# Kernel optimization log

Hardware: AMD Instinct MI355X
Metric: run time of the kernel (lower is better)

Reference implementation:

```python
import jax, jax.numpy as jnp
import numpy as np

C = 16          # cardinality (hard-coded in GraphHead)
E = 1024        # node_encoding_size == representation_size (residual requires equality)
S = 1024        # spatial_head output size (hard-coded Linear(256,1024))
R = 1024        # representation_size
D = R // C      # sub_repr_size = 64
NS, NO = 64, 256
NUM_ITER = 2
EPS = 1e-5


def _w(key, shape, fan_in):
    return jax.random.normal(key, shape, dtype=jnp.float32) * np.float32((2.0 / fan_in) ** 0.5)


def setup_inputs() -> dict:
    key = jax.random.key(0)
    ks = jax.random.split(key, 16)
    inp = {
        'h': jax.random.normal(ks[0], (NS, E), dtype=jnp.float32),
        'o': jax.random.normal(ks[1], (NO, E), dtype=jnp.float32),
        'spatial': jax.random.normal(ks[2], (NS, NO, S), dtype=jnp.float32),
        # attention_head: MultiBranchFusion(2E, 1024, R, 16)
        'att_w1': _w(ks[3], (C, 2 * E, D), 2 * E), 'att_b1': jnp.zeros((C, D), jnp.float32),
        'att_w2': _w(ks[4], (C, S, D), S),         'att_b2': jnp.zeros((C, D), jnp.float32),
        'att_w3': _w(ks[5], (C, D, R), D),         'att_b3': jnp.zeros((C, R), jnp.float32),
        # sub_to_obj: MessageMBF(E, 1024, R, 'subject', 16)
        's2o_w1': _w(ks[6], (C, E, D), E),         's2o_b1': jnp.zeros((C, D), jnp.float32),
        's2o_w2': _w(ks[7], (C, S, D), S),         's2o_b2': jnp.zeros((C, D), jnp.float32),
        's2o_w3': _w(ks[8], (C, D, R), D),         's2o_b3': jnp.zeros((C, R), jnp.float32),
        # obj_to_sub: MessageMBF(E, 1024, R, 'object', 16)
        'o2s_w1': _w(ks[9], (C, E, D), E),         'o2s_b1': jnp.zeros((C, D), jnp.float32),
        'o2s_w2': _w(ks[10], (C, S, D), S),        'o2s_b2': jnp.zeros((C, D), jnp.float32),
        'o2s_w3': _w(ks[11], (C, D, R), D),        'o2s_b3': jnp.zeros((C, R), jnp.float32),
        # adjacency: Linear(R, 1)
        'adj_w': _w(ks[12], (R, 1), R), 'adj_b': jnp.zeros((1,), jnp.float32),
        # LayerNorms
        'ns_g': jnp.ones((E,), jnp.float32), 'ns_b': jnp.zeros((E,), jnp.float32),
        'no_g': jnp.ones((E,), jnp.float32), 'no_b': jnp.zeros((E,), jnp.float32),
    }
    return inp


def _layernorm(x, g, b):
    m = jnp.mean(x, axis=-1, keepdims=True)
    v = jnp.mean((x - m) ** 2, axis=-1, keepdims=True)
    return (x - m) * jax.lax.rsqrt(v + EPS) * g + b


def _mbf_pair(app, spa, w1, b1, w2, b2, w3, b3):
    # app [ns,no,A], spa [ns,no,S] -> [ns,no,R]; sum over C branches of fc3(relu(fc1*fc2))
    a = jnp.einsum('ija,cad->cijd', app, w1) + b1[:, None, None, :]
    s = jnp.einsum('ijs,csd->cijd', spa, w2) + b2[:, None, None, :]
    g = jax.nn.relu(a * s)
    return jnp.einsum('cijd,cdr->ijr', g, w3) + b3.sum(0)


def _msg_subject(h, spa, w1, b1, w2, b2, w3, b3):
    # MessageMBF subject: broadcast fc1(h) [ns,d] against fc2(spa) [ns,no,d]
    a = jnp.einsum('ia,cad->cid', h, w1) + b1[:, None, :]
    s = jnp.einsum('ijs,csd->cijd', spa, w2) + b2[:, None, None, :]
    g = jax.nn.relu(a[:, :, None, :] * s)
    return jnp.einsum('cijd,cdr->ijr', g, w3) + b3.sum(0)  # [ns,no,R]


def _msg_object(o, spa, w1, b1, w2, b2, w3, b3):
    # MessageMBF object: broadcast fc1(o) [no,d] against fc2(spa) [ns,no,d]
    a = jnp.einsum('ja,cad->cjd', o, w1) + b1[:, None, :]
    s = jnp.einsum('ijs,csd->cijd', spa, w2) + b2[:, None, None, :]
    g = jax.nn.relu(a[:, None, :, :] * s)
    return jnp.einsum('cijd,cdr->ijr', g, w3) + b3.sum(0)  # [ns,no,R]


def reference(h, o, spatial,
              att_w1, att_b1, att_w2, att_b2, att_w3, att_b3,
              s2o_w1, s2o_b1, s2o_w2, s2o_b2, s2o_w3, s2o_b3,
              o2s_w1, o2s_b1, o2s_w2, o2s_b2, o2s_w3, o2s_b3,
              adj_w, adj_b, ns_g, ns_b, no_g, no_b):
    ns, no = h.shape[0], o.shape[0]
    for _ in range(NUM_ITER):
        # edge weights via attention MBF on concatenated pair encodings
        pair_app = jnp.concatenate([
            jnp.broadcast_to(h[:, None, :], (ns, no, E)),
            jnp.broadcast_to(o[None, :, :], (ns, no, E)),
        ], axis=-1)
        w = jax.nn.relu(_mbf_pair(pair_app, spatial, att_w1, att_b1, att_w2, att_b2, att_w3, att_b3))
        adj = jnp.einsum('ijr,rk->ij', w, adj_w) + adj_b[0]  # [ns,no]
        # update subject nodes from object messages
        m_o2s = _msg_object(o, spatial, o2s_w1, o2s_b1, o2s_w2, o2s_b2, o2s_w3, o2s_b3)
        msg_h = jax.nn.relu(jnp.einsum('ij,ijr->ir', jax.nn.softmax(adj, axis=1), m_o2s))
        h = _layernorm(h + msg_h, ns_g, ns_b)
        # update object nodes from (updated) subject messages
        m_s2o = _msg_subject(h, spatial, s2o_w1, s2o_b1, s2o_w2, s2o_b2, s2o_w3, s2o_b3)
        msg_o = jax.nn.relu(jnp.einsum('ij,ijr->jr', jax.nn.softmax(adj, axis=0), m_s2o))
        o = _layernorm(o + msg_o, no_g, no_b)
    return jnp.concatenate([h, o], axis=0)  # [ns+no, E]
```

## Files before the change

### kernel.cpp

```cpp
#include <hip/hip_runtime.h>
#include <cstdint>
#include <cstddef>

typedef _Float16 hf;
typedef _Float16 h8v __attribute__((ext_vector_type(8)));
typedef float f4v __attribute__((ext_vector_type(4)));

#define NS 64
#define NO 256
#define MP 16384
#define KD 1024

__device__ __forceinline__ h8v cvt8(float4 a, float4 b) {
    h8v r;
    r[0] = (hf)a.x; r[1] = (hf)a.y; r[2] = (hf)a.z; r[3] = (hf)a.w;
    r[4] = (hf)b.x; r[5] = (hf)b.y; r[6] = (hf)b.z; r[7] = (hf)b.w;
    return r;
}
__device__ __forceinline__ float f4at(const float4& a, const float4& b, int e) {
    const float* p = e < 4 ? (const float*)&a : (const float*)&b;
    return p[e & 3];
}

__global__ void k_pack16(const float* __restrict__ src, hf* __restrict__ dst, int n8) {
    int g = blockIdx.x * 256 + threadIdx.x;
    if (g >= n8) return;
    const float4* s4 = (const float4*)src;
    float4 a = s4[2 * g], b = s4[2 * g + 1];
    *(h8v*)(dst + (size_t)g * 8) = cvt8(a, b);
}

struct RoR { const float* src; hf* dhi; hf* dlo; int Asrc; int aOff; };
struct RoRs { RoR r[7]; };
__global__ void k_reorder16b(RoRs RR) {
    const RoR rt = RR.r[blockIdx.z];
    __shared__ float tile[64][65];
    int c = blockIdx.x, a0 = blockIdx.y * 64;
    int t = threadIdx.x, lx = t & 63, ly = t >> 6;
#pragma unroll
    for (int p = 0; p < 16; ++p) {
        int ar = ly + p * 4;
        tile[ar][lx] = rt.src[(size_t)(c * rt.Asrc + rt.aOff + a0 + ar) * 64 + lx];
    }
    __syncthreads();
#pragma unroll
    for (int p = 0; p < 16; ++p) {
        int d = ly + p * 4;
        float v = tile[lx][d];
        hf h = (hf)v;
        size_t idx = (size_t)(c * 64 + d) * 1024 + a0 + lx;
        rt.dhi[idx] = h;
        if (rt.dlo) rt.dlo[idx] = (hf)(v - (float)h);
    }
}

struct TrR { const float* src; hf* dhi; hf* dlo; };
struct TrRs { TrR r[3]; };
__global__ void k_transpose16b(TrRs RR) {
    const TrR rt = RR.r[blockIdx.z];
    __shared__ float tile[64][65];
    int r0 = blockIdx.x * 64, s0 = blockIdx.y * 64;
    int t = threadIdx.x, lx = t & 63, ly = t >> 6;
#pragma unroll
    for (int p = 0; p < 16; ++p) {
        int srow = ly + p * 4;
        tile[srow][lx] = rt.src[(size_t)(s0 + srow) * 1024 + r0 + lx];
    }
    __syncthreads();
#pragma unroll
    for (int p = 0; p < 16; ++p) {
        int rr = ly + p * 4;
        float v = tile[lx][rr];
        hf h = (hf)v;
        size_t idx = (size_t)(r0 + rr) * 1024 + s0 + lx;
        rt.dhi[idx] = h;
        if (rt.dlo) rt.dlo[idx] = (hf)(v - (float)h);
    }
}

__global__ void k_prep_bc(const float* __restrict__ ab2, const float* __restrict__ ob2,
                          const float* __restrict__ sb2, const float* __restrict__ ab3,
                          const float* __restrict__ ob3, const float* __restrict__ sb3,
                          float* __restrict__ b2cat, float* __restrict__ b3a,
                          float* __restrict__ b3o, float* __restrict__ b3s) {
    int g = blockIdx.x * 256 + threadIdx.x;
    if (g >= 1024) return;
    b2cat[g] = ab2[g]; b2cat[1024 + g] = ob2[g]; b2cat[2048 + g] = sb2[g];
    float sa = 0.f, so = 0.f, ss = 0.f;
    for (int c = 0; c < 16; ++c) {
        sa += ab3[c * 1024 + g];
        so += ob3[c * 1024 + g];
        ss += sb3[c * 1024 + g];
    }
    b3a[g] = sa; b3o[g] = so; b3s[g] = ss;
}

__global__ void k_init_ho(const float* __restrict__ h, const float* __restrict__ o,
                          float* __restrict__ outbuf, hf* __restrict__ h16, hf* __restrict__ o16) {
    int g = blockIdx.x * 256 + threadIdx.x;
    if (g < NS * KD) { float v = h[g]; outbuf[g] = v; h16[g] = (hf)v; }
    int g2 = g - NS * KD;
    if (g2 >= 0 && g2 < NO * KD) { float v = o[g2]; outbuf[NS * KD + g2] = v; o16[g2] = (hf)v; }
}

__global__ __launch_bounds__(256, 2) void k_prep_gemm(
    const hf* __restrict__ sp16,
    const hf* __restrict__ Wah, const hf* __restrict__ Wal,
    const hf* __restrict__ Wo2, const hf* __restrict__ Ws2,
    const float* __restrict__ b2cat,
    hf* __restrict__ Sh, hf* __restrict__ Sl,
    hf* __restrict__ So, hf* __restrict__ Ss) {
    __shared__ hf Ah[4096];
    __shared__ hf Bh[8192];
    __shared__ hf Bl[8192];
    const int tid = threadIdx.x;
    int lin = blockIdx.y * 12 + blockIdx.x;
    int xcd = lin & 7, slot = lin >> 3;
    int xn = slot % 12;
    const int m0 = ((xcd << 4) + slot / 12) * 128;
    const int plane = xn >> 2;
    const int nbase = (xn & 3) * 256;
    const hf* Bb = plane == 0 ? Wah : (plane == 1 ? Wo2 : Ws2);
    const bool hasL = (plane == 0);
    const int lane = tid & 63, wid = tid >> 6;
    const int wm = wid >> 1, wn = wid & 1;
    const int lr = lane & 15, lg = lane >> 4;
    const int srow = tid >> 2, sseg = tid & 3;
    const int wo_ = srow * 32 + (sseg ^ ((srow >> 1) & 3)) * 8;
    const int rsl = (lg ^ ((lr >> 1) & 3)) * 8;

    f4v acc[2][4][4];
    f4v zz; zz[0] = 0.f; zz[1] = 0.f; zz[2] = 0.f; zz[3] = 0.f;
#pragma unroll
    for (int u = 0; u < 2; ++u)
#pragma unroll
        for (int a = 0; a < 4; ++a)
#pragma unroll
            for (int b = 0; b < 4; ++b) acc[u][a][b] = zz;

    const int ko = sseg * 8;
    const hf* pa0 = sp16 + (size_t)(m0 + srow) * KD + ko;
    const hf* pa1 = sp16 + (size_t)(m0 + 64 + srow) * KD + ko;
    const hf* pb00 = Bb + (size_t)(nbase + srow) * KD + ko;
    const hf* pb01 = Bb + (size_t)(nbase + 64 + srow) * KD + ko;
    const hf* pb10 = Bb + (size_t)(nbase + 128 + srow) * KD + ko;
    const hf* pb11 = Bb + (size_t)(nbase + 192 + srow) * KD + ko;
    const hf* ql00 = Wal + (size_t)(nbase + srow) * KD + ko;
    const hf* ql01 = Wal + (size_t)(nbase + 64 + srow) * KD + ko;
    const hf* ql10 = Wal + (size_t)(nbase + 128 + srow) * KD + ko;
    const hf* ql11 = Wal + (size_t)(nbase + 192 + srow) * KD + ko;

    h8v va0, va1, vb00, vb01, vb10, vb11, wb00, wb01, wb10, wb11;
    auto LOAD = [&](int kk) {
        va0 = *(const h8v*)(pa0 + kk); va1 = *(const h8v*)(pa1 + kk);
        vb00 = *(const h8v*)(pb00 + kk); vb01 = *(const h8v*)(pb01 + kk);
        vb10 = *(const h8v*)(pb10 + kk); vb11 = *(const h8v*)(pb11 + kk);
        if (hasL) {
            wb00 = *(const h8v*)(ql00 + kk); wb01 = *(const h8v*)(ql01 + kk);
            wb10 = *(const h8v*)(ql10 + kk); wb11 = *(const h8v*)(ql11 + kk);
        }
    };
    LOAD(0);
    for (int t = 0; t < 32; ++t) {
        __syncthreads();
        *(h8v*)(Ah + wo_) = va0; *(h8v*)(Ah + 2048 + wo_) = va1;
        *(h8v*)(Bh + wo_) = vb00; *(h8v*)(Bh + 2048 + wo_) = vb01;
        *(h8v*)(Bh + 4096 + wo_) = vb10; *(h8v*)(Bh + 6144 + wo_) = vb11;
        if (hasL) {
            *(h8v*)(Bl + wo_) = wb00; *(h8v*)(Bl + 2048 + wo_) = wb01;
            *(h8v*)(Bl + 4096 + wo_) = wb10; *(h8v*)(Bl + 6144 + wo_) = wb11;
        }
        __syncthreads();
        if (t + 1 < 32) LOAD((t + 1) * 32);
        h8v fa[4], fb[4];
#pragma unroll
        for (int x = 0; x < 4; ++x)
            fa[x] = *(const h8v*)(Ah + (wm * 64 + x * 16 + lr) * 32 + rsl);
#pragma unroll
        for (int u = 0; u < 2; ++u) {
#pragma unroll
            for (int x = 0; x < 4; ++x)
                fb[x] = *(const h8v*)(Bh + u * 4096 + (wn * 64 + x * 16 + lr) * 32 + rsl);
#pragma unroll
            for (int mi = 0; mi < 4; ++mi)
#pragma unroll
                for (int ni = 0; ni < 4; ++ni)
                    acc[u][mi][ni] = __builtin_amdgcn_mfma_f32_16x16x32_f16(fa[mi], fb[ni], acc[u][mi][ni], 0, 0, 0);
            if (hasL) {
#pragma unroll
                for (int x = 0; x < 4; ++x)
                    fb[x] = *(const h8v*)(Bl + u * 4096 + (wn * 64 + x * 16 + lr) * 32 + rsl);
#pragma unroll
                for (int mi = 0; mi < 4; ++mi)
#pragma unroll
                    for (int ni = 0; ni < 4; ++ni)
                        acc[u][mi][ni] = __builtin_amdgcn_mfma_f32_16x16x32_f16(fa[mi], fb[ni], acc[u][mi][ni], 0, 0, 0);
            }
        }
    }
#pragma unroll
    for (int u = 0; u < 2; ++u)
#pragma unroll
        for (int mi = 0; mi < 4; ++mi)
#pragma unroll
            for (int ni = 0; ni < 4; ++ni)
#pragma unroll
                for (int r = 0; r < 4; ++r) {
                    int gr = m0 + wm * 64 + mi * 16 + lg * 4 + r;
                    int col = nbase + u * 128 + wn * 64 + ni * 16 + lr;
                    float v = acc[u][mi][ni][r] + b2cat[plane * 1024 + col];
                    size_t idx = (size_t)gr * KD + col;
                    if (plane == 0) {
                        hf hi = (hf)v;
                        Sh[idx] = hi; Sl[idx] = (hf)(v - (float)hi);
                    } else if (plane == 1) So[idx] = (hf)v;
                    else Ss[idx] = (hf)v;
                }
}

__global__ void k_build_g(const hf* __restrict__ Sh, const hf* __restrict__ Sl,
                          const float* __restrict__ e1, const float* __restrict__ e2,
                          hf* __restrict__ Gh, hf* __restrict__ Gl) {
    int g = blockIdx.x * 256 + threadIdx.x;
    size_t base = (size_t)g * 8;
    int m = (int)(base >> 10);
    int k = (int)(base & 1023);
    int i = m >> 8, j = m & 255;
    h8v sh = *(const h8v*)(Sh + base);
    h8v sl = *(const h8v*)(Sl + base);
    float4 ex0 = *(const float4*)(e1 + (size_t)i * KD + k);
    float4 ex1 = *(const float4*)(e1 + (size_t)i * KD + k + 4);
    float4 ey0 = *(const float4*)(e2 + (size_t)j * KD + k);
    float4 ey1 = *(const float4*)(e2 + (size_t)j * KD + k + 4);
    h8v gh, gl;
#pragma unroll
    for (int e = 0; e < 8; ++e) {
        float s = (float)sh[e] + (float)sl[e];
        float ee = f4at(ex0, ex1, e) + f4at(ey0, ey1, e);
        float gg = ee * s; gg = gg > 0.f ? gg : 0.f;
        hf hi = (hf)gg; gh[e] = hi; gl[e] = (hf)(gg - (float)hi);
    }
    *(h8v*)(Gh + base) = gh;
    *(h8v*)(Gl + base) = gl;
}

__global__ __launch_bounds__(256, 2) void k_adj_gemm(
    const hf* __restrict__ Gh, const hf* __restrict__ Gl,
    const hf* __restrict__ W3h, const hf* __restrict__ W3l,
    const float* __restrict__ b3, const float* __restrict__ aw,
    float* __restrict__ adjv) {
    __shared__ hf Ah[4096];
    __shared__ hf Al[4096];
    __shared__ hf Bh[8192];
    __shared__ hf Bl[8192];
    const int tid = threadIdx.x;
    int lin = blockIdx.y * 4 + blockIdx.x;
    int xcd = lin & 7, slot = lin >> 3;
    const int nbase = (slot & 3) * 256;
    const int m0 = ((xcd << 4) + (slot >> 2)) * 128;
    const int lane = tid & 63, wid = tid >> 6;
    const int wm = wid >> 1, wn = wid & 1;
    const int lr = lane & 15, lg = lane >> 4;
    const int srow = tid >> 2, sseg = tid & 3;
    const int wo_ = srow * 32 + (sseg ^ ((srow >> 1) & 3)) * 8;
    const int rsl = (lg ^ ((lr >> 1) & 3)) * 8;
    const int ar0 = m0 + srow, ar1 = ar0 + 64;
    const int ko = sseg * 8;

    f4v acc[2][4][4];
    f4v zz; zz[0] = 0.f; zz[1] = 0.f; zz[2] = 0.f; zz[3] = 0.f;
#pragma unroll
    for (int u = 0; u < 2; ++u)
#pragma unroll
        for (int a = 0; a < 4; ++a)
#pragma unroll
            for (int b = 0; b < 4; ++b) acc[u][a][b] = zz;

    h8v va0, va1, ua0, ua1;
    h8v vb00, vb01, vb10, vb11, wb00, wb01, wb10, wb11;
    auto LOAD = [&](int kk) {
        va0 = *(const h8v*)(Gh + (size_t)ar0 * KD + ko + kk);
        va1 = *(const h8v*)(Gh + (size_t)ar1 * KD + ko + kk);
        ua0 = *(const h8v*)(Gl + (size_t)ar0 * KD + ko + kk);
        ua1 = *(const h8v*)(Gl + (size_t)ar1 * KD + ko + kk);
        vb00 = *(const h8v*)(W3h + (size_t)(nbase + srow) * KD + ko + kk);
        vb01 = *(const h8v*)(W3h + (size_t)(nbase + 64 + srow) * KD + ko + kk);
        vb10 = *(const h8v*)(W3h + (size_t)(nbase + 128 + srow) * KD + ko + kk);
        vb11 = *(const h8v*)(W3h + (size_t)(nbase + 192 + srow) * KD + ko + kk);
        wb00 = *(const h8v*)(W3l + (size_t)(nbase + srow) * KD + ko + kk);
        wb01 = *(const h8v*)(W3l + (size_t)(nbase + 64 + srow) * KD + ko + kk);
        wb10 = *(const h8v*)(W3l + (size_t)(nbase + 128 + srow) * KD + ko + kk);
        wb11 = *(const h8v*)(W3l + (size_t)(nbase + 192 + srow) * KD + ko + kk);
    };
    LOAD(0);
    for (int t = 0; t < 32; ++t) {
        __syncthreads();
        *(h8v*)(Ah + wo_) = va0; *(h8v*)(Ah + 2048 + wo_) = va1;
        *(h8v*)(Al + wo_) = ua0; *(h8v*)(Al + 2048 + wo_) = ua1;
        *(h8v*)(Bh + wo_) = vb00; *(h8v*)(Bh + 2048 + wo_) = vb01;
        *(h8v*)(Bh + 4096 + wo_) = vb10; *(h8v*)(Bh + 6144 + wo_) = vb11;
        *(h8v*)(Bl + wo_) = wb00; *(h8v*)(Bl + 2048 + wo_) = wb01;
        *(h8v*)(Bl + 4096 + wo_) = wb10; *(h8v*)(Bl + 6144 + wo_) = wb11;
        __syncthreads();
        if (t + 1 < 32) LOAD((t + 1) * 32);
        h8v fa[4], fal[4], fb[4];
#pragma unroll
        for (int x = 0; x < 4; ++x) {
            fa[x]  = *(const h8v*)(Ah + (wm * 64 + x * 16 + lr) * 32 + rsl);
            fal[x] = *(const h8v*)(Al + (wm * 64 + x * 16 + lr) * 32 + rsl);
        }
#pragma unroll
        for (int u = 0; u < 2; ++u) {
#pragma unroll
            for (int x = 0; x < 4; ++x)
                fb[x] = *(const h8v*)(Bh + u * 4096 + (wn * 64 + x * 16 + lr) * 32 + rsl);
#pragma unroll
            for (int mi = 0; mi < 4; ++mi)
#pragma unroll
                for (int ni = 0; ni < 4; ++ni)
                    acc[u][mi][ni] = __builtin_amdgcn_mfma_f32_16x16x32_f16(fa[mi], fb[ni], acc[u][mi][ni], 0, 0, 0);
#pragma unroll
            for (int mi = 0; mi < 4; ++mi)
#pragma unroll
                for (int ni = 0; ni < 4; ++ni)
                    acc[u][mi][ni] = __builtin_amdgcn_mfma_f32_16x16x32_f16(fal[mi], fb[ni], acc[u][mi][ni], 0, 0, 0);
#pragma unroll
            for (int x = 0; x < 4; ++x)
                fb[x] = *(const h8v*)(Bl + u * 4096 + (wn * 64 + x * 16 + lr) * 32 + rsl);
#pragma unroll
            for (int mi = 0; mi < 4; ++mi)
#pragma unroll
                for (int ni = 0; ni < 4; ++ni)
                    acc[u][mi][ni] = __builtin_amdgcn_mfma_f32_16x16x32_f16(fa[mi], fb[ni], acc[u][mi][ni], 0, 0, 0);
        }
    }
    float b3v[2][4], awv[2][4];
#pragma unroll
    for (int u = 0; u < 2; ++u)
#pragma unroll
        for (int ni = 0; ni < 4; ++ni) {
            int gc = nbase + u * 128 + wn * 64 + ni * 16 + lr;
            b3v[u][ni] = b3[gc]; awv[u][ni] = aw[gc];
        }
#pragma unroll
    for (int mi = 0; mi < 4; ++mi)
#pragma unroll
        for (int r = 0; r < 4; ++r) {
            float part = 0.f;
#pragma unroll
            for (int u = 0; u < 2; ++u)
#pragma unroll
                for (int ni = 0; ni < 4; ++ni) {
                    float w = acc[u][mi][ni][r] + b3v[u][ni];
                    w = w > 0.f ? w : 0.f;
                    part += w * awv[u][ni];
                }
            part += __shfl_xor(part, 1);
            part += __shfl_xor(part, 2);
            part += __shfl_xor(part, 4);
            part += __shfl_xor(part, 8);
            if (lr == 0) atomicAdd(adjv + m0 + wm * 64 + mi * 16 + lg * 4 + r, part);
        }
}

struct SRoute { const hf* A; const hf* Bh; const hf* Bl; float* C; const float* bias; int m0; int M; };
struct SRoutes { SRoute r[5]; };

__global__ __launch_bounds__(256) void k_small(SRoutes RR) {
    const SRoute rt = RR.r[blockIdx.y];
    __shared__ hf Ah[4096];
    __shared__ hf Bh[4096];
    __shared__ hf Bl[4096];
    const int tid = threadIdx.x;
    const int n0 = blockIdx.x * 128;
    const int kbeg = blockIdx.z * 128;
    const int lane = tid & 63, wid = tid >> 6;
    const int wm = wid >> 1, wn = wid & 1;
    const int lr = lane & 15, lg = lane >> 4;
    const int srow = tid >> 2, sseg = tid & 3;
    const int wo_ = srow * 32 + (sseg ^ ((srow >> 1) & 3)) * 8;
    const int rsl = (lg ^ ((lr >> 1) & 3)) * 8;
    int ar0 = rt.m0 + srow;      if (ar0 >= rt.M) ar0 = rt.M - 1;
    int ar1 = rt.m0 + 64 + srow; if (ar1 >= rt.M) ar1 = rt.M - 1;
    const bool hasL = rt.Bl != nullptr;
    const int ko = kbeg + sseg * 8;

    f4v acc[4][4];
    f4v zz; zz[0] = 0.f; zz[1] = 0.f; zz[2] = 0.f; zz[3] = 0.f;
#pragma unroll
    for (int a = 0; a < 4; ++a)
#pragma unroll
        for (int b = 0; b < 4; ++b) acc[a][b] = zz;

    h8v va0, va1, vb0, vb1, wb0, wb1;
    auto LOAD = [&](int kk) {
        va0 = *(const h8v*)(rt.A + (size_t)ar0 * KD + ko + kk);
        va1 = *(const h8v*)(rt.A + (size_t)ar1 * KD + ko + kk);
        vb0 = *(const h8v*)(rt.Bh + (size_t)(n0 + srow) * KD + ko + kk);
        vb1 = *(const h8v*)(rt.Bh + (size_t)(n0 + 64 + srow) * KD + ko + kk);
        if (hasL) {
            wb0 = *(const h8v*)(rt.Bl + (size_t)(n0 + srow) * KD + ko + kk);
            wb1 = *(const h8v*)(rt.Bl + (size_t)(n0 + 64 + srow) * KD + ko + kk);
        }
    };
    LOAD(0);
    for (int t = 0; t < 4; ++t) {
        __syncthreads();
        *(h8v*)(Ah + wo_) = va0; *(h8v*)(Ah + 2048 + wo_) = va1;
        *(h8v*)(Bh + wo_) = vb0; *(h8v*)(Bh + 2048 + wo_) = vb1;
        if (hasL) { *(h8v*)(Bl + wo_) = wb0; *(h8v*)(Bl + 2048 + wo_) = wb1; }
        __syncthreads();
        if (t + 1 < 4) LOAD((t + 1) * 32);
        h8v fa[4], fb[4];
#pragma unroll
        for (int x = 0; x < 4; ++x) {
            fa[x] = *(const h8v*)(Ah + (wm * 64 + x * 16 + lr) * 32 + rsl);
            fb[x] = *(const h8v*)(Bh + (wn * 64 + x * 16 + lr) * 32 + rsl);
        }
#pragma unroll
        for (int mi = 0; mi < 4; ++mi)
#pragma unroll
            for (int ni = 0; ni < 4; ++ni)
                acc[mi][ni] = __builtin_amdgcn_mfma_f32_16x16x32_f16(fa[mi], fb[ni], acc[mi][ni], 0, 0, 0);
        if (hasL) {
#pragma unroll
            for (int x = 0; x < 4; ++x)
                fb[x] = *(const h8v*)(Bl + (wn * 64 + x * 16 + lr) * 32 + rsl);
#pragma unroll
            for (int mi = 0; mi < 4; ++mi)
#pragma unroll
                for (int ni = 0; ni < 4; ++ni)
                    acc[mi][ni] = __builtin_amdgcn_mfma_f32_16x16x32_f16(fa[mi], fb[ni], acc[mi][ni], 0, 0, 0);
        }
    }
#pragma unroll
    for (int mi = 0; mi < 4; ++mi)
#pragma unroll
        for (int ni = 0; ni < 4; ++ni)
#pragma unroll
            for (int r = 0; r < 4; ++r) {
                int gr = rt.m0 + wm * 64 + mi * 16 + lg * 4 + r;
                int gc = n0 + wn * 64 + ni * 16 + lr;
                if (gr < rt.M) {
                    float v = acc[mi][ni][r];
                    if (rt.bias && blockIdx.z == 0) v += rt.bias[gc];
                    atomicAdd(rt.C + (size_t)gr * KD + gc, v);
                }
            }
}

__global__ void k_softmax_rows(const float* __restrict__ adj, float* __restrict__ p) {
    __shared__ float red[256];
    int i = blockIdx.x, j = threadIdx.x;
    float x = adj[i * 256 + j];
    red[j] = x; __syncthreads();
    for (int s = 128; s > 0; s >>= 1) { if (j < s) red[j] = fmaxf(red[j], red[j + s]); __syncthreads(); }
    float mx = red[0]; __syncthreads();
    float e = __expf(x - mx);
    red[j] = e; __syncthreads();
    for (int s = 128; s > 0; s >>= 1) { if (j < s) red[j] += red[j + s]; __syncthreads(); }
    p[i * 256 + j] = e / red[0];
}

__global__ void k_softmax_cols(const float* __restrict__ adj, float* __restrict__ q) {
    int j = blockIdx.x, i = threadIdx.x;
    float x = adj[i * 256 + j];
    float mx = x;
#pragma unroll
    for (int off = 32; off > 0; off >>= 1) mx = fmaxf(mx, __shfl_xor(mx, off));
    float e = __expf(x - mx);
    float s = e;
#pragma unroll
    for (int off = 32; off > 0; off >>= 1) s += __shfl_xor(s, off);
    q[i * 256 + j] = e / s;
}

__global__ void k_build_Gh(const hf* __restrict__ S, const float* __restrict__ aF,
                           const float* __restrict__ p, hf* __restrict__ Gh) {
    __shared__ float pl[256];
    int i = blockIdx.x;
    int k = blockIdx.y * 256 + threadIdx.x;
    pl[threadIdx.x] = p[i * 256 + threadIdx.x];
    __syncthreads();
    const hf* sp = S + (size_t)(i * 256) * KD + k;
    float acc = 0.f;
#pragma unroll 4
    for (int j = 0; j < 256; ++j) {
        float a = aF[(size_t)j * KD + k];
        float s = (float)sp[(size_t)j * KD];
        float g = a * s; g = g > 0.f ? g : 0.f;
        acc += pl[j] * g;
    }
    Gh[(size_t)i * KD + k] = (hf)acc;
}

__global__ void k_build_Go(const hf* __restrict__ S, const float* __restrict__ aF,
                           const float* __restrict__ q, hf* __restrict__ Go) {
    __shared__ float ql[64];
    int j = blockIdx.x;
    int k = blockIdx.y * 256 + threadIdx.x;
    if (threadIdx.x < 64) ql[threadIdx.x] = q[threadIdx.x * 256 + j];
    __syncthreads();
    const hf* sp = S + (size_t)j * KD + k;
    float acc = 0.f;
#pragma unroll 4
    for (int i = 0; i < 64; ++i) {
        float a = aF[(size_t)i * KD + k];
        float s = (float)sp[(size_t)(i * 256) * KD];
        float g = a * s; g = g > 0.f ? g : 0.f;
        acc += ql[i] * g;
    }
    Go[(size_t)j * KD + k] = (hf)acc;
}

__global__ void k_ln_update(float* __restrict__ x, const float* __restrict__ msg,
                            const float* __restrict__ b3, const float* __restrict__ gamma,
                            const float* __restrict__ beta, hf* __restrict__ x16) {
    __shared__ float red[256];
    int r = blockIdx.x, t = threadIdx.x;
    float v[4];
    float s = 0.f;
#pragma unroll
    for (int e = 0; e < 4; ++e) {
        int idx = t + e * 256;
        float mm = msg[(size_t)r * KD + idx] + b3[idx];
        mm = mm > 0.f ? mm : 0.f;
        v[e] = x[(size_t)r * KD + idx] + mm;
        s += v[e];
    }
    red[t] = s; __syncthreads();
    for (int st = 128; st > 0; st >>= 1) { if (t < st) red[t] += red[t + st]; __syncthreads(); }
    float mean = red[0] * (1.f / 1024.f);
    __syncthreads();
    float s2 = 0.f;
#pragma unroll
    for (int e = 0; e < 4; ++e) { float d = v[e] - mean; s2 += d * d; }
    red[t] = s2; __syncthreads();
    for (int st = 128; st > 0; st >>= 1) { if (t < st) red[t] += red[t + st]; __syncthreads(); }
    float var = red[0] * (1.f / 1024.f);
    float rstd = rsqrtf(var + 1e-5f);
#pragma unroll
    for (int e = 0; e < 4; ++e) {
        int idx = t + e * 256;
        float y = (v[e] - mean) * rstd * gamma[idx] + beta[idx];
        x[(size_t)r * KD + idx] = y;
        x16[(size_t)r * KD + idx] = (hf)y;
    }
}

extern "C" void kernel_launch(void* const* d_in, const int* in_sizes, int n_in,
                              void* d_out, int out_size, void* d_ws, size_t ws_size,
                              hipStream_t stream) {
    const float* h_in    = (const float*)d_in[0];
    const float* o_in    = (const float*)d_in[1];
    const float* spatial = (const float*)d_in[2];
    const float* att_w1  = (const float*)d_in[3];
    const float* att_b1  = (const float*)d_in[4];
    const float* att_w2  = (const float*)d_in[5];
    const float* att_b2  = (const float*)d_in[6];
    const float* att_w3  = (const float*)d_in[7];
    const float* att_b3  = (const float*)d_in[8];
    const float* s2o_w1  = (const float*)d_in[9];
    const float* s2o_b1  = (const float*)d_in[10];
    const float* s2o_w2  = (const float*)d_in[11];
    const float* s2o_b2  = (const float*)d_in[12];
    const float* s2o_w3  = (const float*)d_in[13];
    const float* s2o_b3  = (const float*)d_in[14];
    const float* o2s_w1  = (const float*)d_in[15];
    const float* o2s_b1  = (const float*)d_in[16];
    const float* o2s_w2  = (const float*)d_in[17];
    const float* o2s_b2  = (const float*)d_in[18];
    const float* o2s_w3  = (const float*)d_in[19];
    const float* o2s_b3  = (const float*)d_in[20];
    const float* adj_w   = (const float*)d_in[21];
    const float* ns_g    = (const float*)d_in[23];
    const float* ns_b    = (const float*)d_in[24];
    const float* no_g    = (const float*)d_in[25];
    const float* no_b    = (const float*)d_in[26];

    char* ws = (char*)d_ws;
    size_t off = 0;
    auto alloc = [&](size_t bytes) -> char* {
        char* pp = ws + off;
        off += (bytes + 255) & ~(size_t)255;
        return pp;
    };
    const size_t PLANE = (size_t)MP * KD * sizeof(hf);
    const size_t WMAT  = (size_t)1024 * 1024 * sizeof(hf);
    hf* S_att_h = (hf*)alloc(PLANE);
    hf* S_att_l = (hf*)alloc(PLANE);
    hf* S_o2s   = (hf*)alloc(PLANE);
    hf* S_s2o   = (hf*)alloc(PLANE);
    hf* gA_h    = (hf*)alloc(PLANE);
    hf* gA_l    = (hf*)alloc(PLANE);
    hf* sp16    = gA_h;
    hf* W2att_h = (hf*)alloc(WMAT); hf* W2att_l = (hf*)alloc(WMAT);
    hf* W2o2s   = (hf*)alloc(WMAT);
    hf* W2s2o   = (hf*)alloc(WMAT);
    hf* W1ah_h  = (hf*)alloc(WMAT); hf* W1ah_l  = (hf*)alloc(WMAT);
    hf* W1ao_h  = (hf*)alloc(WMAT); hf* W1ao_l  = (hf*)alloc(WMAT);
    hf* W1o2s   = (hf*)alloc(WMAT);
    hf* W1s2o   = (hf*)alloc(WMAT);
    hf* W3a_h   = (hf*)alloc(WMAT); hf* W3a_l   = (hf*)alloc(WMAT);
    hf* W3o     = (hf*)alloc(WMAT);
    hf* W3s     = (hf*)alloc(WMAT);
    float* b2cat = (float*)alloc(3072 * 4);
    float* b3a   = (float*)alloc(1024 * 4);
    float* b3o   = (float*)alloc(1024 * 4);
    float* b3s   = (float*)alloc(1024 * 4);
    float* fc1h = (float*)alloc((size_t)NS * KD * 4);
    float* fc1o = (float*)alloc((size_t)NO * KD * 4);
    float* aO2S = (float*)alloc((size_t)NO * KD * 4);
    float* aS2O = (float*)alloc((size_t)NS * KD * 4);
    float* msgh = (float*)alloc((size_t)NS * KD * 4);
    float* msgo = (float*)alloc((size_t)NO * KD * 4);
    float* adjv = (float*)alloc((size_t)MP * 4);
    char* zend_ = (char*)(adjv + MP);
    size_t zlen = (size_t)(zend_ - (char*)fc1h);
    float* pbuf = (float*)alloc((size_t)MP * 4);
    float* qbuf = (float*)alloc((size_t)MP * 4);
    hf* h16 = (hf*)alloc((size_t)NS * KD * sizeof(hf));
    hf* o16 = (hf*)alloc((size_t)NO * KD * sizeof(hf));
    hf* Gh  = (hf*)alloc((size_t)NS * KD * sizeof(hf));
    hf* Go  = (hf*)alloc((size_t)NO * KD * sizeof(hf));

    float* hbuf = (float*)d_out;
    float* obuf = (float*)d_out + NS * KD;

    k_pack16<<<dim3(MP * KD / 8 / 256), 256, 0, stream>>>(spatial, sp16, MP * KD / 8);
    {
        RoRs R;
        R.r[0] = { att_w2, W2att_h, W2att_l, 1024, 0 };
        R.r[1] = { o2s_w2, W2o2s, nullptr, 1024, 0 };
        R.r[2] = { s2o_w2, W2s2o, nullptr, 1024, 0 };
        R.r[3] = { att_w1, W1ah_h, W1ah_l, 2048, 0 };
        R.r[4] = { att_w1, W1ao_h, W1ao_l, 2048, 1024 };
        R.r[5] = { o2s_w1, W1o2s, nullptr, 1024, 0 };
        R.r[6] = { s2o_w1, W1s2o, nullptr, 1024, 0 };
        k_reorder16b<<<dim3(16, 16, 7), 256, 0, stream>>>(R);
    }
    {
        TrRs T;
        T.r[0] = { att_w3, W3a_h, W3a_l };
        T.r[1] = { o2s_w3, W3o, nullptr };
        T.r[2] = { s2o_w3, W3s, nullptr };
        k_transpose16b<<<dim3(16, 16, 3), 256, 0, stream>>>(T);
    }
    k_prep_bc<<<dim3(4), 256, 0, stream>>>(att_b2, o2s_b2, s2o_b2, att_b3, o2s_b3, s2o_b3,
                                           b2cat, b3a, b3o, b3s);
    k_init_ho<<<dim3(1280), 256, 0, stream>>>(h_in, o_in, (float*)d_out, h16, o16);
    k_prep_gemm<<<dim3(12, 128), 256, 0, stream>>>(sp16, W2att_h, W2att_l, W2o2s, W2s2o,
                                                   b2cat, S_att_h, S_att_l, S_o2s, S_s2o);

    for (int it = 0; it < 2; ++it) {
        hipMemsetAsync(fc1h, 0, zlen, stream);
        {
            SRoutes R;
            R.r[0] = { h16, W1ah_h, W1ah_l, fc1h, att_b1, 0,   NS };
            R.r[1] = { o16, W1ao_h, W1ao_l, fc1o, nullptr, 0,   NO };
            R.r[2] = { o16, W1ao_h, W1ao_l, fc1o, nullptr, 128, NO };
            R.r[3] = { o16, W1o2s,  nullptr, aO2S, o2s_b1, 0,   NO };
            R.r[4] = { o16, W1o2s,  nullptr, aO2S, o2s_b1, 128, NO };
            k_small<<<dim3(8, 5, 8), 256, 0, stream>>>(R);
        }
        k_build_g<<<dim3(MP * KD / 8 / 256), 256, 0, stream>>>(S_att_h, S_att_l, fc1h, fc1o, gA_h, gA_l);
        k_adj_gemm<<<dim3(4, 128), 256, 0, stream>>>(gA_h, gA_l, W3a_h, W3a_l, b3a, adj_w, adjv);
        k_softmax_rows<<<dim3(NS), 256, 0, stream>>>(adjv, pbuf);
        k_softmax_cols<<<dim3(NO), 64, 0, stream>>>(adjv, qbuf);
        k_build_Gh<<<dim3(NS, 4), 256, 0, stream>>>(S_o2s, aO2S, pbuf, Gh);
        {
            SRoutes R;
            R.r[0] = { Gh, W3o, nullptr, msgh, nullptr, 0, NS };
            k_small<<<dim3(8, 1, 8), 256, 0, stream>>>(R);
        }
        k_ln_update<<<dim3(NS), 256, 0, stream>>>(hbuf, msgh, b3o, ns_g, ns_b, h16);
        {
            SRoutes R;
            R.r[0] = { h16, W1s2o, nullptr, aS2O, s2o_b1, 0, NS };
            k_small<<<dim3(8, 1, 8), 256, 0, stream>>>(R);
        }
        k_build_Go<<<dim3(NO, 4), 256, 0, stream>>>(S_s2o, aS2O, qbuf, Go);
        {
            SRoutes R;
            R.r[0] = { Go, W3s, nullptr, msgo, nullptr, 0,   NO };
            R.r[1] = { Go, W3s, nullptr, msgo, nullptr, 128, NO };
            k_small<<<dim3(8, 2, 8), 256, 0, stream>>>(R);
        }
        k_ln_update<<<dim3(NO), 256, 0, stream>>>(obuf, msgo, b3s, no_g, no_b, o16);
    }
    (void)in_sizes; (void)n_in; (void)out_size; (void)ws_size;
}
```

Baseline: 682.3 us.

## Double-buffer B tiles in LDS and load A fragments straight from global

In both the prep GEMM and the adjacency GEMM, the A operand is no longer staged through shared memory; each wave loads its MFMA A fragments directly from global memory. The B tiles are double-buffered in LDS, so each iteration needs one barrier instead of two and the next tile's store overlaps the current compute. This cuts LDS traffic and synchronisation, but A fragment loads are now uncoalesced per-row global reads issued right before use, which can expose latency. LDS use per block goes up.

```diff
diff --git a/kernel.cpp b/kernel.cpp
--- a/kernel.cpp
+++ b/kernel.cpp
@@ -110,9 +110,8 @@
     const float* __restrict__ b2cat,
     hf* __restrict__ Sh, hf* __restrict__ Sl,
     hf* __restrict__ So, hf* __restrict__ Ss) {
-    __shared__ hf Ah[4096];
-    __shared__ hf Bh[8192];
-    __shared__ hf Bl[8192];
+    __shared__ hf Bh[2][8192];
+    __shared__ hf Bl[2][8192];
     const int tid = threadIdx.x;
     int lin = blockIdx.y * 12 + blockIdx.x;
     int xcd = lin & 7, slot = lin >> 3;
@@ -139,8 +138,6 @@
             for (int b = 0; b < 4; ++b) acc[u][a][b] = zz;
 
     const int ko = sseg * 8;
-    const hf* pa0 = sp16 + (size_t)(m0 + srow) * KD + ko;
-    const hf* pa1 = sp16 + (size_t)(m0 + 64 + srow) * KD + ko;
     const hf* pb00 = Bb + (size_t)(nbase + srow) * KD + ko;
     const hf* pb01 = Bb + (size_t)(nbase + 64 + srow) * KD + ko;
     const hf* pb10 = Bb + (size_t)(nbase + 128 + srow) * KD + ko;
@@ -149,10 +146,13 @@
     const hf* ql01 = Wal + (size_t)(nbase + 64 + srow) * KD + ko;
     const hf* ql10 = Wal + (size_t)(nbase + 128 + srow) * KD + ko;
     const hf* ql11 = Wal + (size_t)(nbase + 192 + srow) * KD + ko;
-
-    h8v va0, va1, vb00, vb01, vb10, vb11, wb00, wb01, wb10, wb11;
-    auto LOAD = [&](int kk) {
-        va0 = *(const h8v*)(pa0 + kk); va1 = *(const h8v*)(pa1 + kk);
+    const hf* pA[4];
+#pragma unroll
+    for (int mi = 0; mi < 4; ++mi)
+        pA[mi] = sp16 + (size_t)(m0 + wm * 64 + mi * 16 + lr) * KD + lg * 8;
+
+    h8v vb00, vb01, vb10, vb11, wb00, wb01, wb10, wb11;
+    auto LOADB = [&](int kk) {
         vb00 = *(const h8v*)(pb00 + kk); vb01 = *(const h8v*)(pb01 + kk);
         vb10 = *(const h8v*)(pb10 + kk); vb11 = *(const h8v*)(pb11 + kk);
         if (hasL) {
@@ -160,27 +160,31 @@
             wb10 = *(const h8v*)(ql10 + kk); wb11 = *(const h8v*)(ql11 + kk);
         }
     };
-    LOAD(0);
+    auto STOREB = [&](int b) {
+        hf* B = Bh[b]; hf* BL = Bl[b];
+        *(h8v*)(B + wo_) = vb00; *(h8v*)(B + 2048 + wo_) = vb01;
+        *(h8v*)(B + 4096 + wo_) = vb10; *(h8v*)(B + 6144 + wo_) = vb11;
+        if (hasL) {
+            *(h8v*)(BL + wo_) = wb00; *(h8v*)(BL + 2048 + wo_) = wb01;
+            *(h8v*)(BL + 4096 + wo_) = wb10; *(h8v*)(BL + 6144 + wo_) = wb11;
+        }
+    };
+    LOADB(0);
+    STOREB(0);
+    __syncthreads();
     for (int t = 0; t < 32; ++t) {
-        __syncthreads();
-        *(h8v*)(Ah + wo_) = va0; *(h8v*)(Ah + 2048 + wo_) = va1;
-        *(h8v*)(Bh + wo_) = vb00; *(h8v*)(Bh + 2048 + wo_) = vb01;
-        *(h8v*)(Bh + 4096 + wo_) = vb10; *(h8v*)(Bh + 6144 + wo_) = vb11;
-        if (hasL) {
-            *(h8v*)(Bl + wo_) = wb00; *(h8v*)(Bl + 2048 + wo_) = wb01;
-            *(h8v*)(Bl + 4096 + wo_) = wb10; *(h8v*)(Bl + 6144 + wo_) = wb11;
-        }
-        __syncthreads();
-        if (t + 1 < 32) LOAD((t + 1) * 32);
-        h8v fa[4], fb[4];
-#pragma unroll
-        for (int x = 0; x < 4; ++x)
-            fa[x] = *(const h8v*)(Ah + (wm * 64 + x * 16 + lr) * 32 + rsl);
+        const int cur = t & 1;
+        if (t < 31) LOADB((t + 1) * 32);
+        h8v fa[4];
+#pragma unroll
+        for (int mi = 0; mi < 4; ++mi) fa[mi] = *(const h8v*)(pA[mi] + t * 32);
+        const hf* B = Bh[cur]; const hf* BL = Bl[cur];
+        h8v fb[4];
 #pragma unroll
         for (int u = 0; u < 2; ++u) {
 #pragma unroll
             for (int x = 0; x < 4; ++x)
-                fb[x] = *(const h8v*)(Bh + u * 4096 + (wn * 64 + x * 16 + lr) * 32 + rsl);
+                fb[x] = *(const h8v*)(B + u * 4096 + (wn * 64 + x * 16 + lr) * 32 + rsl);
 #pragma unroll
             for (int mi = 0; mi < 4; ++mi)
 #pragma unroll
@@ -189,7 +193,7 @@
             if (hasL) {
 #pragma unroll
                 for (int x = 0; x < 4; ++x)
-                    fb[x] = *(const h8v*)(Bl + u * 4096 + (wn * 64 + x * 16 + lr) * 32 + rsl);
+                    fb[x] = *(const h8v*)(BL + u * 4096 + (wn * 64 + x * 16 + lr) * 32 + rsl);
 #pragma unroll
                 for (int mi = 0; mi < 4; ++mi)
 #pragma unroll
@@ -197,6 +201,8 @@
                         acc[u][mi][ni] = __builtin_amdgcn_mfma_f32_16x16x32_f16(fa[mi], fb[ni], acc[u][mi][ni], 0, 0, 0);
             }
         }
+        if (t < 31) STOREB(cur ^ 1);
+        __syncthreads();
     }
 #pragma unroll
     for (int u = 0; u < 2; ++u)
@@ -249,10 +255,8 @@
     const hf* __restrict__ W3h, const hf* __restrict__ W3l,
     const float* __restrict__ b3, const float* __restrict__ aw,
     float* __restrict__ adjv) {
-    __shared__ hf Ah[4096];
-    __shared__ hf Al[4096];
-    __shared__ hf Bh[8192];
-    __shared__ hf Bl[8192];
+    __shared__ hf Bh2[2][8192];
+    __shared__ hf Bl2[2][8192];
     const int tid = threadIdx.x;
     int lin = blockIdx.y * 4 + blockIdx.x;
     int xcd = lin & 7, slot = lin >> 3;
@@ -264,7 +268,6 @@
     const int srow = tid >> 2, sseg = tid & 3;
     const int wo_ = srow * 32 + (sseg ^ ((srow >> 1) & 3)) * 8;
     const int rsl = (lg ^ ((lr >> 1) & 3)) * 8;
-    const int ar0 = m0 + srow, ar1 = ar0 + 64;
     const int ko = sseg * 8;
 
     f4v acc[2][4][4];
@@ -276,44 +279,54 @@
 #pragma unroll
             for (int b = 0; b < 4; ++b) acc[u][a][b] = zz;
 
-    h8v va0, va1, ua0, ua1;
+    const hf* pb00 = W3h + (size_t)(nbase + srow) * KD + ko;
+    const hf* pb01 = W3h + (size_t)(nbase + 64 + srow) * KD + ko;
+    const hf* pb10 = W3h + (size_t)(nbase + 128 + srow) * KD + ko;
+    const hf* pb11 = W3h + (size_t)(nbase + 192 + srow) * KD + ko;
+    const hf* ql00 = W3l + (size_t)(nbase + srow) * KD + ko;
+    const hf* ql01 = W3l + (size_t)(nbase + 64 + srow) * KD + ko;
+    const hf* ql10 = W3l + (size_t)(nbase + 128 + srow) * KD + ko;
+    const hf* ql11 = W3l + (size_t)(nbase + 192 + srow) * KD + ko;
+    const hf* pAh[4]; const hf* pAl[4];
+#pragma unroll
+    for (int mi = 0; mi < 4; ++mi) {
+        size_t roff = (size_t)(m0 + wm * 64 + mi * 16 + lr) * KD + lg * 8;
+        pAh[mi] = Gh + roff; pAl[mi] = Gl + roff;
+    }
+
     h8v vb00, vb01, vb10, vb11, wb00, wb01, wb10, wb11;
-    auto LOAD = [&](int kk) {
-        va0 = *(const h8v*)(Gh + (size_t)ar0 * KD + ko + kk);
-        va1 = *(const h8v*)(Gh + (size_t)ar1 * KD + ko + kk);
-        ua0 = *(const h8v*)(Gl + (size_t)ar0 * KD + ko + kk);
-        ua1 = *(const h8v*)(Gl + (size_t)ar1 * KD + ko + kk);
-        vb00 = *(const h8v*)(W3h + (size_t)(nbase + srow) * KD + ko + kk);
-        vb01 = *(const h8v*)(W3h + (size_t)(nbase + 64 + srow) * KD + ko + kk);
-        vb10 = *(const h8v*)(W3h + (size_t)(nbase + 128 + srow) * KD + ko + kk);
-        vb11 = *(const h8v*)(W3h + (size_t)(nbase + 192 + srow) * KD + ko + kk);
-        wb00 = *(const h8v*)(W3l + (size_t)(nbase + srow) * KD + ko + kk);
-        wb01 = *(const h8v*)(W3l + (size_t)(nbase + 64 + srow) * KD + ko + kk);
-        wb10 = *(const h8v*)(W3l + (size_t)(nbase + 128 + srow) * KD + ko + kk);
-        wb11 = *(const h8v*)(W3l + (size_t)(nbase + 192 + srow) * KD + ko + kk);
+    auto LOADB = [&](int kk) {
+        vb00 = *(const h8v*)(pb00 + kk); vb01 = *(const h8v*)(pb01 + kk);
+        vb10 = *(const h8v*)(pb10 + kk); vb11 = *(const h8v*)(pb11 + kk);
+        wb00 = *(const h8v*)(ql00 + kk); wb01 = *(const h8v*)(ql01 + kk);
+        wb10 = *(const h8v*)(ql10 + kk); wb11 = *(const h8v*)(ql11 + kk);
     };
-    LOAD(0);
+    auto STOREB = [&](int b) {
+        hf* B = Bh2[b]; hf* BL = Bl2[b];
+        *(h8v*)(B + wo_) = vb00; *(h8v*)(B + 2048 + wo_) = vb01;
+        *(h8v*)(B + 4096 + wo_) = vb10; *(h8v*)(B + 6144 + wo_) = vb11;
+        *(h8v*)(BL + wo_) = wb00; *(h8v*)(BL + 2048 + wo_) = wb01;
+        *(h8v*)(BL + 4096 + wo_) = wb10; *(h8v*)(BL + 6144 + wo_) = wb11;
+    };
+    LOADB(0);
+    STOREB(0);
+    __syncthreads();
     for (int t = 0; t < 32; ++t) {
-        __syncthreads();
-        *(h8v*)(Ah + wo_) = va0; *(h8v*)(Ah + 2048 + wo_) = va1;
-        *(h8v*)(Al + wo_) = ua0; *(h8v*)(Al + 2048 + wo_) = ua1;
-        *(h8v*)(Bh + wo_) = vb00; *(h8v*)(Bh + 2048 + wo_) = vb01;
-        *(h8v*)(Bh + 4096 + wo_) = vb10; *(h8v*)(Bh + 6144 + wo_) = vb11;
-        *(h8v*)(Bl + wo_) = wb00; *(h8v*)(Bl + 2048 + wo_) = wb01;
-        *(h8v*)(Bl + 4096 + wo_) = wb10; *(h8v*)(Bl + 6144 + wo_) = wb11;
-        __syncthreads();
-        if (t + 1 < 32) LOAD((t + 1) * 32);
-        h8v fa[4], fal[4], fb[4];
-#pragma unroll
-        for (int x = 0; x < 4; ++x) {
-            fa[x]  = *(const h8v*)(Ah + (wm * 64 + x * 16 + lr) * 32 + rsl);
-            fal[x] = *(const h8v*)(Al + (wm * 64 + x * 16 + lr) * 32 + rsl);
-        }
+        const int cur = t & 1;
+        if (t < 31) LOADB((t + 1) * 32);
+        h8v fa[4], fal[4];
+#pragma unroll
+        for (int mi = 0; mi < 4; ++mi) {
+            fa[mi]  = *(const h8v*)(pAh[mi] + t * 32);
+            fal[mi] = *(const h8v*)(pAl[mi] + t * 32);
+        }
+        const hf* B = Bh2[cur]; const hf* BL = Bl2[cur];
+        h8v fb[4];
 #pragma unroll
         for (int u = 0; u < 2; ++u) {
 #pragma unroll
             for (int x = 0; x < 4; ++x)
-                fb[x] = *(const h8v*)(Bh + u * 4096 + (wn * 64 + x * 16 + lr) * 32 + rsl);
+                fb[x] = *(const h8v*)(B + u * 4096 + (wn * 64 + x * 16 + lr) * 32 + rsl);
 #pragma unroll
             for (int mi = 0; mi < 4; ++mi)
 #pragma unroll
@@ -326,13 +339,15 @@
                     acc[u][mi][ni] = __builtin_amdgcn_mfma_f32_16x16x32_f16(fal[mi], fb[ni], acc[u][mi][ni], 0, 0, 0);
 #pragma unroll
             for (int x = 0; x < 4; ++x)
-                fb[x] = *(const h8v*)(Bl + u * 4096 + (wn * 64 + x * 16 + lr) * 32 + rsl);
+                fb[x] = *(const h8v*)(BL + u * 4096 + (wn * 64 + x * 16 + lr) * 32 + rsl);
 #pragma unroll
             for (int mi = 0; mi < 4; ++mi)
 #pragma unroll
                 for (int ni = 0; ni < 4; ++ni)
                     acc[u][mi][ni] = __builtin_amdgcn_mfma_f32_16x16x32_f16(fa[mi], fb[ni], acc[u][mi][ni], 0, 0, 0);
         }
+        if (t < 31) STOREB(cur ^ 1);
+        __syncthreads();
     }
     float b3v[2][4], awv[2][4];
 #pragma unroll
```

Measured after the change: 742.6 us. 1.09x slower.

## Double-buffer B tiles in LDS and load A fragments directly from global

Applied to the files above, without the earlier changes.

In the prep GEMM, the B tiles are now double-buffered in shared memory, so only one barrier per k-step is needed instead of two. The A operand no longer goes through LDS: each wave loads its MFMA fragments straight from global memory into registers, prefetched one step ahead. This removes the A staging stores and reads and overlaps the next B store with compute. In exchange, LDS use grows (two B buffers, 64KB total), which may limit occupancy. A global loads are also less coalesced and duplicated across the two wn waves.

```diff
diff --git a/kernel.cpp b/kernel.cpp
--- a/kernel.cpp
+++ b/kernel.cpp
@@ -110,9 +110,8 @@
     const float* __restrict__ b2cat,
     hf* __restrict__ Sh, hf* __restrict__ Sl,
     hf* __restrict__ So, hf* __restrict__ Ss) {
-    __shared__ hf Ah[4096];
-    __shared__ hf Bh[8192];
-    __shared__ hf Bl[8192];
+    __shared__ hf Bhs[2][8192];
+    __shared__ hf Bls[2][8192];
     const int tid = threadIdx.x;
     int lin = blockIdx.y * 12 + blockIdx.x;
     int xcd = lin & 7, slot = lin >> 3;
@@ -139,8 +138,6 @@
             for (int b = 0; b < 4; ++b) acc[u][a][b] = zz;
 
     const int ko = sseg * 8;
-    const hf* pa0 = sp16 + (size_t)(m0 + srow) * KD + ko;
-    const hf* pa1 = sp16 + (size_t)(m0 + 64 + srow) * KD + ko;
     const hf* pb00 = Bb + (size_t)(nbase + srow) * KD + ko;
     const hf* pb01 = Bb + (size_t)(nbase + 64 + srow) * KD + ko;
     const hf* pb10 = Bb + (size_t)(nbase + 128 + srow) * KD + ko;
@@ -149,10 +146,13 @@
     const hf* ql01 = Wal + (size_t)(nbase + 64 + srow) * KD + ko;
     const hf* ql10 = Wal + (size_t)(nbase + 128 + srow) * KD + ko;
     const hf* ql11 = Wal + (size_t)(nbase + 192 + srow) * KD + ko;
-
-    h8v va0, va1, vb00, vb01, vb10, vb11, wb00, wb01, wb10, wb11;
-    auto LOAD = [&](int kk) {
-        va0 = *(const h8v*)(pa0 + kk); va1 = *(const h8v*)(pa1 + kk);
+    const hf* pA[4];
+#pragma unroll
+    for (int mi = 0; mi < 4; ++mi)
+        pA[mi] = sp16 + (size_t)(m0 + wm * 64 + mi * 16 + lr) * KD + lg * 8;
+
+    h8v vb00, vb01, vb10, vb11, wb00, wb01, wb10, wb11;
+    auto LOADB = [&](int kk) {
         vb00 = *(const h8v*)(pb00 + kk); vb01 = *(const h8v*)(pb01 + kk);
         vb10 = *(const h8v*)(pb10 + kk); vb11 = *(const h8v*)(pb11 + kk);
         if (hasL) {
@@ -160,27 +160,38 @@
             wb10 = *(const h8v*)(ql10 + kk); wb11 = *(const h8v*)(ql11 + kk);
         }
     };
-    LOAD(0);
+    auto STOREB = [&](int b) {
+        hf* B = Bhs[b]; hf* BL = Bls[b];
+        *(h8v*)(B + wo_) = vb00; *(h8v*)(B + 2048 + wo_) = vb01;
+        *(h8v*)(B + 4096 + wo_) = vb10; *(h8v*)(B + 6144 + wo_) = vb11;
+        if (hasL) {
+            *(h8v*)(BL + wo_) = wb00; *(h8v*)(BL + 2048 + wo_) = wb01;
+            *(h8v*)(BL + 4096 + wo_) = wb10; *(h8v*)(BL + 6144 + wo_) = wb11;
+        }
+    };
+    h8v fan[4];
+    LOADB(0);
+#pragma unroll
+    for (int mi = 0; mi < 4; ++mi) fan[mi] = *(const h8v*)(pA[mi]);
+    STOREB(0);
+    __syncthreads();
     for (int t = 0; t < 32; ++t) {
-        __syncthreads();
-        *(h8v*)(Ah + wo_) = va0; *(h8v*)(Ah + 2048 + wo_) = va1;
-        *(h8v*)(Bh + wo_) = vb00; *(h8v*)(Bh + 2048 + wo_) = vb01;
-        *(h8v*)(Bh + 4096 + wo_) = vb10; *(h8v*)(Bh + 6144 + wo_) = vb11;
-        if (hasL) {
-            *(h8v*)(Bl + wo_) = wb00; *(h8v*)(Bl + 2048 + wo_) = wb01;
-            *(h8v*)(Bl + 4096 + wo_) = wb10; *(h8v*)(Bl + 6144 + wo_) = wb11;
-        }
-        __syncthreads();
-        if (t + 1 < 32) LOAD((t + 1) * 32);
-        h8v fa[4], fb[4];
-#pragma unroll
-        for (int x = 0; x < 4; ++x)
-            fa[x] = *(const h8v*)(Ah + (wm * 64 + x * 16 + lr) * 32 + rsl);
+        const int cur = t & 1;
+        h8v fa[4];
+#pragma unroll
+        for (int mi = 0; mi < 4; ++mi) fa[mi] = fan[mi];
+        if (t < 31) {
+            LOADB((t + 1) * 32);
+#pragma unroll
+            for (int mi = 0; mi < 4; ++mi) fan[mi] = *(const h8v*)(pA[mi] + (t + 1) * 32);
+        }
+        const hf* B = Bhs[cur]; const hf* BL = Bls[cur];
+        h8v fb[4];
 #pragma unroll
         for (int u = 0; u < 2; ++u) {
 #pragma unroll
             for (int x = 0; x < 4; ++x)
-                fb[x] = *(const h8v*)(Bh + u * 4096 + (wn * 64 + x * 16 + lr) * 32 + rsl);
+                fb[x] = *(const h8v*)(B + u * 4096 + (wn * 64 + x * 16 + lr) * 32 + rsl);
 #pragma unroll
             for (int mi = 0; mi < 4; ++mi)
 #pragma unroll
@@ -189,7 +200,7 @@
             if (hasL) {
 #pragma unroll
                 for (int x = 0; x < 4; ++x)
-                    fb[x] = *(const h8v*)(Bl + u * 4096 + (wn * 64 + x * 16 + lr) * 32 + rsl);
+                    fb[x] = *(const h8v*)(BL + u * 4096 + (wn * 64 + x * 16 + lr) * 32 + rsl);
 #pragma unroll
                 for (int mi = 0; mi < 4; ++mi)
 #pragma unroll
@@ -197,6 +208,8 @@
                         acc[u][mi][ni] = __builtin_amdgcn_mfma_f32_16x16x32_f16(fa[mi], fb[ni], acc[u][mi][ni], 0, 0, 0);
             }
         }
+        if (t < 31) STOREB(cur ^ 1);
+        __syncthreads();
     }
 #pragma unroll
     for (int u = 0; u < 2; ++u)
```

Measured after the change: 707.3 us. 1.04x slower.
